# Kernel tuning notes

Measured on AMD Instinct MI355X. Metric: run time of the kernel, lower is better.

Reference implementation:

```python
import jax, jax.numpy as jnp
import numpy as np

CONF_THRES = 0.25
IOU_THRES = 0.45
MAX_DET = 1000
MAX_WH = 4096.0   # class offset for per-class NMS (yolov5 trick)
TOPK = 2048       # pre-NMS candidate cap (fixed-shape stand-in for max_nms)


def _xywh2xyxy(b):
    cx, cy, w, h = b[..., 0], b[..., 1], b[..., 2], b[..., 3]
    return jnp.stack([cx - w * 0.5, cy - h * 0.5, cx + w * 0.5, cy + h * 0.5], axis=-1)


def _box_iou(a, b):
    # a, b: [K, 4] in xyxy -> [K, K] pairwise IoU
    lt = jnp.maximum(a[:, None, :2], b[None, :, :2])
    rb = jnp.minimum(a[:, None, 2:], b[None, :, 2:])
    wh = jnp.clip(rb - lt, 0.0)
    inter = wh[..., 0] * wh[..., 1]
    area_a = (a[:, 2] - a[:, 0]) * (a[:, 3] - a[:, 1])
    area_b = (b[:, 2] - b[:, 0]) * (b[:, 3] - b[:, 1])
    return inter / (area_a[:, None] + area_b[None, :] - inter + 1e-7)


def _nms_single(pred):
    # pred: [N, 5+C] = (cx, cy, w, h, obj, cls...)
    obj = pred[:, 4]
    cls_prob = pred[:, 5:]
    cls_conf = jnp.max(cls_prob, axis=-1)
    cls_id = jnp.argmax(cls_prob, axis=-1)
    score = obj * cls_conf                      # conf = obj_conf * cls_conf (best class)
    valid = (obj > CONF_THRES) & (score > CONF_THRES)
    score = jnp.where(valid, score, 0.0)
    boxes = _xywh2xyxy(pred[:, :4])

    # keep top-K candidates by confidence (sorted descending)
    tops, idx = jax.lax.top_k(score, TOPK)
    boxes_k = boxes[idx]                        # [K, 4]
    cls_k = cls_id[idx]                         # [K]
    val_k = tops > 0.0

    # per-class NMS via class offset
    shifted = boxes_k + (cls_k.astype(boxes_k.dtype) * MAX_WH)[:, None]
    iou = _box_iou(shifted, shifted)            # [K, K]

    j = jnp.arange(TOPK)

    def body(i, keep):
        # if box i survives, suppress lower-scored boxes with IoU > thresh
        sup = keep[i] & (iou[i] > IOU_THRES) & (j > i)
        return keep & ~sup

    keep = jax.lax.fori_loop(0, TOPK, body, val_k)

    # gather up to MAX_DET kept detections (already score-sorted)
    fs, fi = jax.lax.top_k(jnp.where(keep, tops, -1.0), MAX_DET)
    ok = fs > 0.0
    det_boxes = jnp.where(ok[:, None], boxes_k[fi], 0.0)
    det_score = jnp.where(ok, tops[fi], 0.0)
    det_cls = jnp.where(ok, cls_k[fi].astype(det_boxes.dtype), -1.0)
    # [MAX_DET, 6] = (x1, y1, x2, y2, conf, cls); padded rows have conf 0, cls -1
    return jnp.concatenate([det_boxes, det_score[:, None], det_cls[:, None]], axis=-1)


def setup_inputs() -> dict:
    key = jax.random.key(0)
    raw = jax.random.uniform(key, (16, 25200, 85), dtype=jnp.float32)
    xy = raw[..., 0:2] * 640.0            # centers within a 640x640 image
    wh = raw[..., 2:4] * 120.0 + 2.0      # box sizes in [2, 122]
    rest = raw[..., 4:]                   # obj + class probs in [0, 1)
    pred = jnp.concatenate([xy, wh, rest], axis=-1)
    return {"pred": pred}


def reference(pred):
    return jax.vmap(_nms_single)(pred)
```

## Files before the change

kernel.cpp:

```cpp
#include <hip/hip_runtime.h>
#include <stdint.h>

#pragma clang fp contract(off)

#define BB 16
#define NN 25200
#define ROW 85
#define NCLS 80
#define TK 2048
#define SORTN 4096
#define NBIN 4096
#define MAXDET 1000
#define CONF 0.25f
#define IOUT 0.45f
#define MAXWH 4096.0f
#define SROWS 64

typedef float fvec4 __attribute__((ext_vector_type(4)));

#define AS1 __attribute__((address_space(1)))
#define AS3 __attribute__((address_space(3)))

__global__ __launch_bounds__(64) void score_kernel(const float* __restrict__ pred,
                                                   float* __restrict__ scores,
                                                   int* __restrict__ cls,
                                                   unsigned int* __restrict__ hist) {
  __shared__ __align__(16) float srow[SROWS * ROW];
  const int tile = blockIdx.x;
  const int b = blockIdx.y;
  const int lane = threadIdx.x;
  const int row0 = tile * SROWS;
  int nrows = NN - row0;
  if (nrows > SROWS) nrows = SROWS;
  const char* gsrc = (const char*)(pred + ((size_t)b * NN + row0) * ROW);
  const int nbytes = nrows * ROW * 4;
  for (int off = lane * 16; off < nbytes; off += 64 * 16) {
    __builtin_amdgcn_global_load_lds((AS1 void*)(gsrc + off),
                                     (AS3 void*)((char*)srow + (off - lane * 16)),
                                     16, 0, 0);
  }
  __builtin_amdgcn_s_waitcnt(0);
  __syncthreads();
  if (lane < nrows) {
    const int n = row0 + lane;
    const float* r = srow + lane * ROW;
    float obj = r[4];
    float best = r[5];
    int bid = 0;
#pragma unroll
    for (int c = 1; c < NCLS; ++c) {
      float p = r[5 + c];
      if (p > best) { best = p; bid = c; }
    }
    float score = obj * best;
    bool valid = (obj > CONF) && (score > CONF);
    float sout = valid ? score : 0.0f;
    scores[(size_t)b * NN + n] = sout;
    cls[(size_t)b * NN + n] = bid;
    if (valid) {
      unsigned int u = __float_as_uint(sout);
      unsigned int bin = (u - 0x3E800001u) >> 12;
      if (bin > NBIN - 1) bin = NBIN - 1;
      atomicAdd(&hist[(size_t)b * NBIN + bin], 1u);
    }
  }
}

__global__ __launch_bounds__(1024) void gather_kernel(const float* __restrict__ pred,
                                                      const float* __restrict__ scores,
                                                      const int* __restrict__ cls,
                                                      const unsigned int* __restrict__ hist,
                                                      float* __restrict__ tops,
                                                      float* __restrict__ boxes,
                                                      int* __restrict__ clsk,
                                                      int* __restrict__ keep,
                                                      int* __restrict__ cgrp,
                                                      int* __restrict__ coff) {
  const int b = blockIdx.x;
  const int t = threadIdx.x;
  const int w = t >> 6;
  const int lane = t & 63;
  __shared__ unsigned long long skey[SORTN];
  __shared__ unsigned int sh[NBIN];
  __shared__ unsigned int soff[NBIN];
  __shared__ int spart[1024];
  __shared__ unsigned short scls[TK];
  __shared__ int ccnt[NCLS];
  __shared__ int coffs[NCLS + 1];
  __shared__ int sP;

  if (t == 0) sP = 0;
  for (int i = t; i < NBIN; i += 1024) sh[i] = hist[(size_t)b * NBIN + i];
  for (int i = t; i < SORTN; i += 1024) skey[i] = 0ull;
  __syncthreads();

  int loc[4];
  int ssum = 0;
#pragma unroll
  for (int k = 0; k < 4; ++k) {
    loc[k] = (int)sh[NBIN - 1 - (4 * t + k)];
    ssum += loc[k];
  }
  spart[t] = ssum;
  __syncthreads();
  for (int o = 1; o < 1024; o <<= 1) {
    int v = (t >= o) ? spart[t - o] : 0;
    __syncthreads();
    spart[t] += v;
    __syncthreads();
  }
  int run = spart[t] - ssum;
#pragma unroll
  for (int k = 0; k < 4; ++k) {
    int bin = NBIN - 1 - (4 * t + k);
    soff[bin] = (unsigned int)run;
    if (run < TK && run + loc[k] >= TK) sP = bin;
    run += loc[k];
  }
  __syncthreads();
  const int P = sP;
  for (int i = t; i < NBIN; i += 1024) sh[i] = 0u;
  __syncthreads();

  const float* sc = scores + (size_t)b * NN;
  for (int n = t; n < NN; n += 1024) {
    unsigned int u = __float_as_uint(sc[n]);
    if (u > 0x3E800000u) {
      unsigned int bin = (u - 0x3E800001u) >> 12;
      if (bin > NBIN - 1) bin = NBIN - 1;
      if ((int)bin >= P) {
        unsigned int pos = soff[bin] + atomicAdd(&sh[bin], 1u);
        if (pos < SORTN)
          skey[pos] = ((unsigned long long)u << 32) | (unsigned int)(~n);
      }
    }
  }
  __syncthreads();

  for (int bin = P + w; bin < NBIN; bin += 16) {
    int s = (int)sh[bin];
    if (s < 2) continue;
    int base = (int)soff[bin];
    if (base >= SORTN) continue;
    if (base + s > SORTN) s = SORTN - base;
    if (s < 2) continue;
    if (s <= 64) {
      bool act = lane < s;
      unsigned long long key = act ? skey[base + lane] : 0ull;
      int rank = 0;
      for (int j = 0; j < s; ++j) {
        unsigned long long kj = skey[base + j];
        rank += (act && kj > key) ? 1 : 0;
      }
      if (act) skey[base + rank] = key;
    } else {
      for (int pass = 0; pass < s; ++pass) {
        for (int p = base + (pass & 1) + 2 * lane; p + 1 < base + s; p += 128) {
          unsigned long long a = skey[p], b2 = skey[p + 1];
          if (a < b2) { skey[p] = b2; skey[p + 1] = a; }
        }
        asm volatile("" ::: "memory");
      }
    }
    asm volatile("" ::: "memory");
  }
  __syncthreads();

  for (int i = t; i < TK; i += 1024) {
    unsigned long long key = skey[i];
    unsigned int ub = (unsigned int)(key >> 32);
    size_t gi = (size_t)b * TK + i;
    if (ub == 0u) {
      tops[gi] = 0.0f;
      clsk[gi] = 0;
      keep[gi] = 0;
      fvec4 z; z[0] = 0.f; z[1] = 0.f; z[2] = 0.f; z[3] = 0.f;
      *(fvec4*)(boxes + gi * 4) = z;
      scls[i] = (unsigned short)0xFFFFu;
    } else {
      int idx = (int)(~(unsigned int)key);
      tops[gi] = __uint_as_float(ub);
      int cl = cls[(size_t)b * NN + idx];
      clsk[gi] = cl;
      scls[i] = (unsigned short)cl;
      const float* rowp = pred + ((size_t)b * NN + idx) * ROW;
      float cx = rowp[0], cy = rowp[1], w2 = rowp[2], h2 = rowp[3];
      float hw = w2 * 0.5f, hh = h2 * 0.5f;
      fvec4 bb4;
      bb4[0] = cx - hw; bb4[1] = cy - hh; bb4[2] = cx + hw; bb4[3] = cy + hh;
      *(fvec4*)(boxes + gi * 4) = bb4;
    }
  }
  __syncthreads();

#pragma unroll
  for (int k = 0; k < 5; ++k) {
    int c = w + 16 * k;
    int cnt = 0;
    for (int base2 = 0; base2 < TK; base2 += 64) {
      bool match = ((int)scls[base2 + lane] == c);
      cnt += (int)__popcll(__ballot(match));
    }
    if (lane == 0) ccnt[c] = cnt;
  }
  __syncthreads();
  if (t == 0) {
    int r2 = 0;
    for (int c = 0; c < NCLS; ++c) { coffs[c] = r2; r2 += ccnt[c]; }
    coffs[NCLS] = r2;
  }
  __syncthreads();
#pragma unroll
  for (int k = 0; k < 5; ++k) {
    int c = w + 16 * k;
    int run2 = coffs[c];
    for (int base2 = 0; base2 < TK; base2 += 64) {
      bool match = ((int)scls[base2 + lane] == c);
      unsigned long long bal = __ballot(match);
      int r3 = (int)__popcll(bal & ((1ull << lane) - 1ull));
      if (match) cgrp[(size_t)b * TK + run2 + r3] = base2 + lane;
      run2 += (int)__popcll(bal);
    }
  }
  for (int c = t; c <= NCLS; c += 1024) coff[b * (NCLS + 1) + c] = coffs[c];
}

__global__ __launch_bounds__(64) void nms_kernel(const float* __restrict__ tops,
                                                 const float* __restrict__ boxes,
                                                 const int* __restrict__ cgrp,
                                                 const int* __restrict__ coff,
                                                 int* __restrict__ keep) {
  const int c = blockIdx.x;
  const int b = blockIdx.y;
  const int lane = threadIdx.x;
  const int start = coff[b * (NCLS + 1) + c];
  const int end = coff[b * (NCLS + 1) + c + 1];
  const int m = end - start;
  if (m <= 0) return;
  __shared__ float sx1[TK], sy1[TK], sx2[TK], sy2[TK];
  __shared__ unsigned short spos[TK];
  __shared__ unsigned char skp[TK];

  const float shift = (float)c * MAXWH;
  for (int i = lane; i < m; i += 64) {
    int j = cgrp[(size_t)b * TK + start + i];
    fvec4 bx = *(const fvec4*)(boxes + ((size_t)b * TK + j) * 4);
    sx1[i] = bx[0] + shift;
    sy1[i] = bx[1] + shift;
    sx2[i] = bx[2] + shift;
    sy2[i] = bx[3] + shift;
    spos[i] = (unsigned short)j;
    skp[i] = (tops[(size_t)b * TK + j] > 0.0f) ? 1 : 0;
  }
  __syncthreads();

  for (int i = 0; i < m; ++i) {
    __syncthreads();
    if (!skp[i]) continue;
    float ax1 = sx1[i], ay1 = sy1[i], ax2 = sx2[i], ay2 = sy2[i];
    float aarea = (ax2 - ax1) * (ay2 - ay1);
    for (int j = i + 1 + lane; j < m; j += 64) {
      float bx1 = sx1[j], by1 = sy1[j], bx2 = sx2[j], by2 = sy2[j];
      float ltx = fmaxf(ax1, bx1), lty = fmaxf(ay1, by1);
      float rbx = fminf(ax2, bx2), rby = fminf(ay2, by2);
      float iw = fmaxf(rbx - ltx, 0.0f);
      float ih = fmaxf(rby - lty, 0.0f);
      float inter = iw * ih;
      float barea = (bx2 - bx1) * (by2 - by1);
      float iou = inter / (aarea + barea - inter + 1e-7f);
      if (iou > IOUT) skp[j] = 0;
    }
  }
  __syncthreads();

  for (int i = lane; i < m; i += 64) {
    keep[(size_t)b * TK + spos[i]] = skp[i];
  }
}

__global__ __launch_bounds__(256) void out_kernel(const float* __restrict__ tops,
                                                  const float* __restrict__ boxes,
                                                  const int* __restrict__ clsk,
                                                  const int* __restrict__ keep,
                                                  float* __restrict__ out) {
  int b = blockIdx.x;
  int t = threadIdx.x;
  __shared__ int scnt[256];
  const int CH = TK / 256;
  int base = t * CH;
  int kp[CH];
  int cnt = 0;
  for (int k = 0; k < CH; ++k) {
    kp[k] = keep[(size_t)b * TK + base + k];
    cnt += kp[k];
  }
  scnt[t] = cnt;
  __syncthreads();
  for (int off = 1; off < 256; off <<= 1) {
    int v = (t >= off) ? scnt[t - off] : 0;
    __syncthreads();
    scnt[t] += v;
    __syncthreads();
  }
  int r = scnt[t] - cnt;
  int K = scnt[255];
  for (int k = 0; k < CH; ++k) {
    if (kp[k]) {
      if (r < MAXDET) {
        int j = base + k;
        float* o = out + ((size_t)b * MAXDET + r) * 6;
        const float* bx = boxes + ((size_t)b * TK + j) * 4;
        o[0] = bx[0]; o[1] = bx[1]; o[2] = bx[2]; o[3] = bx[3];
        o[4] = tops[(size_t)b * TK + j];
        o[5] = (float)clsk[(size_t)b * TK + j];
      }
      ++r;
    }
  }
  int Kc = K < MAXDET ? K : MAXDET;
  for (int r2 = Kc + t; r2 < MAXDET; r2 += 256) {
    float* o = out + ((size_t)b * MAXDET + r2) * 6;
    o[0] = 0.0f; o[1] = 0.0f; o[2] = 0.0f; o[3] = 0.0f; o[4] = 0.0f; o[5] = -1.0f;
  }
}

extern "C" void kernel_launch(void* const* d_in, const int* in_sizes, int n_in,
                              void* d_out, int out_size, void* d_ws, size_t ws_size,
                              hipStream_t stream) {
  const float* pred = (const float*)d_in[0];
  float* out = (float*)d_out;

  char* ws = (char*)d_ws;
  size_t off = 0;
  float* scores = (float*)(ws + off); off += (size_t)BB * NN * 4;
  int*   cls    = (int*)(ws + off);   off += (size_t)BB * NN * 4;
  float* tops   = (float*)(ws + off); off += (size_t)BB * TK * 4;
  float* boxes  = (float*)(ws + off); off += (size_t)BB * TK * 16;
  int*   clsk   = (int*)(ws + off);   off += (size_t)BB * TK * 4;
  int*   keep   = (int*)(ws + off);   off += (size_t)BB * TK * 4;
  unsigned int* hist = (unsigned int*)(ws + off); off += (size_t)BB * NBIN * 4;
  int*   cgrp   = (int*)(ws + off);   off += (size_t)BB * TK * 4;
  int*   coff   = (int*)(ws + off);   off += (size_t)BB * (NCLS + 1) * 4;
  (void)ws_size; (void)in_sizes; (void)n_in; (void)out_size;

  hipMemsetAsync(hist, 0, (size_t)BB * NBIN * 4, stream);
  score_kernel<<<dim3((NN + SROWS - 1) / SROWS, BB), 64, 0, stream>>>(pred, scores, cls, hist);
  gather_kernel<<<BB, 1024, 0, stream>>>(pred, scores, cls, hist, tops, boxes, clsk, keep, cgrp, coff);
  nms_kernel<<<dim3(NCLS, BB), 64, 0, stream>>>(tops, boxes, cgrp, coff, keep);
  out_kernel<<<BB, 256, 0, stream>>>(tops, boxes, clsk, keep, out);
}
```

Baseline: 272.6 us.

## Fuse gather, per-class NMS and output into one per-batch kernel

Merges the gather, NMS and output kernels into a single 1024-thread block per image. Candidate boxes, scores, classes and keep flags now stay in LDS instead of going through global workspace buffers. NMS runs per wavefront over its classes, keeping suppression bits in a register mask and fetching the reference box by lane shuffle, so the per-iteration block barrier is gone. The score kernel also uses 128-thread blocks and stores class ids as bytes; in exchange, NMS runs with only 16 blocks and drops the class coordinate shift, which may change rounding slightly.

```diff
diff --git a/kernel.cpp b/kernel.cpp
--- a/kernel.cpp
+++ b/kernel.cpp
@@ -21,29 +21,30 @@
 #define AS1 __attribute__((address_space(1)))
 #define AS3 __attribute__((address_space(3)))
 
-__global__ __launch_bounds__(64) void score_kernel(const float* __restrict__ pred,
-                                                   float* __restrict__ scores,
-                                                   int* __restrict__ cls,
-                                                   unsigned int* __restrict__ hist) {
+__global__ __launch_bounds__(128) void score_kernel(const float* __restrict__ pred,
+                                                    float* __restrict__ scores,
+                                                    uint8_t* __restrict__ cls,
+                                                    unsigned int* __restrict__ hist) {
   __shared__ __align__(16) float srow[SROWS * ROW];
   const int tile = blockIdx.x;
   const int b = blockIdx.y;
-  const int lane = threadIdx.x;
+  const int tid = threadIdx.x;
+  const int lane = tid & 63;
   const int row0 = tile * SROWS;
   int nrows = NN - row0;
   if (nrows > SROWS) nrows = SROWS;
   const char* gsrc = (const char*)(pred + ((size_t)b * NN + row0) * ROW);
   const int nbytes = nrows * ROW * 4;
-  for (int off = lane * 16; off < nbytes; off += 64 * 16) {
+  for (int off = tid * 16; off < nbytes; off += 128 * 16) {
     __builtin_amdgcn_global_load_lds((AS1 void*)(gsrc + off),
                                      (AS3 void*)((char*)srow + (off - lane * 16)),
                                      16, 0, 0);
   }
   __builtin_amdgcn_s_waitcnt(0);
   __syncthreads();
-  if (lane < nrows) {
-    const int n = row0 + lane;
-    const float* r = srow + lane * ROW;
+  if (tid < nrows) {
+    const int n = row0 + tid;
+    const float* r = srow + tid * ROW;
     float obj = r[4];
     float best = r[5];
     int bid = 0;
@@ -56,7 +57,7 @@
     bool valid = (obj > CONF) && (score > CONF);
     float sout = valid ? score : 0.0f;
     scores[(size_t)b * NN + n] = sout;
-    cls[(size_t)b * NN + n] = bid;
+    cls[(size_t)b * NN + n] = (uint8_t)bid;
     if (valid) {
       unsigned int u = __float_as_uint(sout);
       unsigned int bin = (u - 0x3E800001u) >> 12;
@@ -66,16 +67,11 @@
   }
 }
 
-__global__ __launch_bounds__(1024) void gather_kernel(const float* __restrict__ pred,
-                                                      const float* __restrict__ scores,
-                                                      const int* __restrict__ cls,
-                                                      const unsigned int* __restrict__ hist,
-                                                      float* __restrict__ tops,
-                                                      float* __restrict__ boxes,
-                                                      int* __restrict__ clsk,
-                                                      int* __restrict__ keep,
-                                                      int* __restrict__ cgrp,
-                                                      int* __restrict__ coff) {
+__global__ __launch_bounds__(1024) void mega_kernel(const float* __restrict__ pred,
+                                                    const float* __restrict__ scores,
+                                                    const uint8_t* __restrict__ cls,
+                                                    const unsigned int* __restrict__ hist,
+                                                    float* __restrict__ out) {
   const int b = blockIdx.x;
   const int t = threadIdx.x;
   const int w = t >> 6;
@@ -83,8 +79,12 @@
   __shared__ unsigned long long skey[SORTN];
   __shared__ unsigned int sh[NBIN];
   __shared__ unsigned int soff[NBIN];
+  __shared__ float sx1[TK], sy1[TK], sx2[TK], sy2[TK];
+  __shared__ float stop[TK];
+  __shared__ unsigned short scls[TK];
+  __shared__ unsigned short cgrpL[TK];
+  __shared__ unsigned char skp[TK];
   __shared__ int spart[1024];
-  __shared__ unsigned short scls[TK];
   __shared__ int ccnt[NCLS];
   __shared__ int coffs[NCLS + 1];
   __shared__ int sP;
@@ -169,26 +169,20 @@
   for (int i = t; i < TK; i += 1024) {
     unsigned long long key = skey[i];
     unsigned int ub = (unsigned int)(key >> 32);
-    size_t gi = (size_t)b * TK + i;
     if (ub == 0u) {
-      tops[gi] = 0.0f;
-      clsk[gi] = 0;
-      keep[gi] = 0;
-      fvec4 z; z[0] = 0.f; z[1] = 0.f; z[2] = 0.f; z[3] = 0.f;
-      *(fvec4*)(boxes + gi * 4) = z;
+      stop[i] = 0.0f;
       scls[i] = (unsigned short)0xFFFFu;
+      skp[i] = 0;
+      sx1[i] = 0.f; sy1[i] = 0.f; sx2[i] = 0.f; sy2[i] = 0.f;
     } else {
       int idx = (int)(~(unsigned int)key);
-      tops[gi] = __uint_as_float(ub);
-      int cl = cls[(size_t)b * NN + idx];
-      clsk[gi] = cl;
-      scls[i] = (unsigned short)cl;
+      stop[i] = __uint_as_float(ub);
+      scls[i] = (unsigned short)cls[(size_t)b * NN + idx];
+      skp[i] = 1;
       const float* rowp = pred + ((size_t)b * NN + idx) * ROW;
       float cx = rowp[0], cy = rowp[1], w2 = rowp[2], h2 = rowp[3];
       float hw = w2 * 0.5f, hh = h2 * 0.5f;
-      fvec4 bb4;
-      bb4[0] = cx - hw; bb4[1] = cy - hh; bb4[2] = cx + hw; bb4[3] = cy + hh;
-      *(fvec4*)(boxes + gi * 4) = bb4;
+      sx1[i] = cx - hw; sy1[i] = cy - hh; sx2[i] = cx + hw; sy2[i] = cy + hh;
     }
   }
   __syncthreads();
@@ -218,107 +212,101 @@
       bool match = ((int)scls[base2 + lane] == c);
       unsigned long long bal = __ballot(match);
       int r3 = (int)__popcll(bal & ((1ull << lane) - 1ull));
-      if (match) cgrp[(size_t)b * TK + run2 + r3] = base2 + lane;
+      if (match) cgrpL[run2 + r3] = (unsigned short)(base2 + lane);
       run2 += (int)__popcll(bal);
     }
   }
-  for (int c = t; c <= NCLS; c += 1024) coff[b * (NCLS + 1) + c] = coffs[c];
-}
-
-__global__ __launch_bounds__(64) void nms_kernel(const float* __restrict__ tops,
-                                                 const float* __restrict__ boxes,
-                                                 const int* __restrict__ cgrp,
-                                                 const int* __restrict__ coff,
-                                                 int* __restrict__ keep) {
-  const int c = blockIdx.x;
-  const int b = blockIdx.y;
-  const int lane = threadIdx.x;
-  const int start = coff[b * (NCLS + 1) + c];
-  const int end = coff[b * (NCLS + 1) + c + 1];
-  const int m = end - start;
-  if (m <= 0) return;
-  __shared__ float sx1[TK], sy1[TK], sx2[TK], sy2[TK];
-  __shared__ unsigned short spos[TK];
-  __shared__ unsigned char skp[TK];
-
-  const float shift = (float)c * MAXWH;
-  for (int i = lane; i < m; i += 64) {
-    int j = cgrp[(size_t)b * TK + start + i];
-    fvec4 bx = *(const fvec4*)(boxes + ((size_t)b * TK + j) * 4);
-    sx1[i] = bx[0] + shift;
-    sy1[i] = bx[1] + shift;
-    sx2[i] = bx[2] + shift;
-    sy2[i] = bx[3] + shift;
-    spos[i] = (unsigned short)j;
-    skp[i] = (tops[(size_t)b * TK + j] > 0.0f) ? 1 : 0;
-  }
-  __syncthreads();
-
-  for (int i = 0; i < m; ++i) {
+  __syncthreads();
+
+  for (int k = 0; k < 5; ++k) {
+    int c = w + 16 * k;
+    int start = coffs[c];
+    int m = coffs[c + 1] - start;
+    if (m <= 0) continue;
+    int nq = (m + 63) >> 6;
+    unsigned int km = 0;
+    for (int q = 0; q < nq; ++q)
+      if (lane + (q << 6) < m) km |= (1u << q);
+    float b0x1 = 0.f, b0y1 = 0.f, b0x2 = 0.f, b0y2 = 0.f;
+    if (lane < m) {
+      int e0 = cgrpL[start + lane];
+      b0x1 = sx1[e0]; b0y1 = sy1[e0]; b0x2 = sx2[e0]; b0y2 = sy2[e0];
+    }
+    for (int i = 0; i < m; ++i) {
+      int q = i >> 6;
+      unsigned int kmi = __shfl(km, i & 63);
+      if (!((kmi >> q) & 1u)) continue;
+      float ax1, ay1, ax2, ay2;
+      if (q == 0) {
+        ax1 = __shfl(b0x1, i); ay1 = __shfl(b0y1, i);
+        ax2 = __shfl(b0x2, i); ay2 = __shfl(b0y2, i);
+      } else {
+        int ei = cgrpL[start + i];
+        ax1 = sx1[ei]; ay1 = sy1[ei]; ax2 = sx2[ei]; ay2 = sy2[ei];
+      }
+      float aarea = (ax2 - ax1) * (ay2 - ay1);
+      if ((km & 1u) && lane > i) {
+        float ltx = fmaxf(ax1, b0x1), lty = fmaxf(ay1, b0y1);
+        float rbx = fminf(ax2, b0x2), rby = fminf(ay2, b0y2);
+        float iw = fmaxf(rbx - ltx, 0.0f);
+        float ih = fmaxf(rby - lty, 0.0f);
+        float inter = iw * ih;
+        float barea = (b0x2 - b0x1) * (b0y2 - b0y1);
+        float iou = inter / (aarea + barea - inter + 1e-7f);
+        if (iou > IOUT) km &= ~1u;
+      }
+      for (int q2 = 1; q2 < nq; ++q2) {
+        int j = lane + (q2 << 6);
+        if (((km >> q2) & 1u) && j > i && j < m) {
+          int ej = cgrpL[start + j];
+          float jx1 = sx1[ej], jy1 = sy1[ej], jx2 = sx2[ej], jy2 = sy2[ej];
+          float ltx = fmaxf(ax1, jx1), lty = fmaxf(ay1, jy1);
+          float rbx = fminf(ax2, jx2), rby = fminf(ay2, jy2);
+          float iw = fmaxf(rbx - ltx, 0.0f);
+          float ih = fmaxf(rby - lty, 0.0f);
+          float inter = iw * ih;
+          float barea = (jx2 - jx1) * (jy2 - jy1);
+          float iou = inter / (aarea + barea - inter + 1e-7f);
+          if (iou > IOUT) km &= ~(1u << q2);
+        }
+      }
+    }
+    for (int q = 0; q < nq; ++q) {
+      int j = lane + (q << 6);
+      if (j < m) skp[cgrpL[start + j]] = (unsigned char)((km >> q) & 1u);
+    }
+  }
+  __syncthreads();
+
+  int kp0 = (int)skp[2 * t];
+  int kp1 = (int)skp[2 * t + 1];
+  int cnt2 = kp0 + kp1;
+  spart[t] = cnt2;
+  __syncthreads();
+  for (int o = 1; o < 1024; o <<= 1) {
+    int v = (t >= o) ? spart[t - o] : 0;
     __syncthreads();
-    if (!skp[i]) continue;
-    float ax1 = sx1[i], ay1 = sy1[i], ax2 = sx2[i], ay2 = sy2[i];
-    float aarea = (ax2 - ax1) * (ay2 - ay1);
-    for (int j = i + 1 + lane; j < m; j += 64) {
-      float bx1 = sx1[j], by1 = sy1[j], bx2 = sx2[j], by2 = sy2[j];
-      float ltx = fmaxf(ax1, bx1), lty = fmaxf(ay1, by1);
-      float rbx = fminf(ax2, bx2), rby = fminf(ay2, by2);
-      float iw = fmaxf(rbx - ltx, 0.0f);
-      float ih = fmaxf(rby - lty, 0.0f);
-      float inter = iw * ih;
-      float barea = (bx2 - bx1) * (by2 - by1);
-      float iou = inter / (aarea + barea - inter + 1e-7f);
-      if (iou > IOUT) skp[j] = 0;
-    }
-  }
-  __syncthreads();
-
-  for (int i = lane; i < m; i += 64) {
-    keep[(size_t)b * TK + spos[i]] = skp[i];
-  }
-}
-
-__global__ __launch_bounds__(256) void out_kernel(const float* __restrict__ tops,
-                                                  const float* __restrict__ boxes,
-                                                  const int* __restrict__ clsk,
-                                                  const int* __restrict__ keep,
-                                                  float* __restrict__ out) {
-  int b = blockIdx.x;
-  int t = threadIdx.x;
-  __shared__ int scnt[256];
-  const int CH = TK / 256;
-  int base = t * CH;
-  int kp[CH];
-  int cnt = 0;
-  for (int k = 0; k < CH; ++k) {
-    kp[k] = keep[(size_t)b * TK + base + k];
-    cnt += kp[k];
-  }
-  scnt[t] = cnt;
-  __syncthreads();
-  for (int off = 1; off < 256; off <<= 1) {
-    int v = (t >= off) ? scnt[t - off] : 0;
+    spart[t] += v;
     __syncthreads();
-    scnt[t] += v;
-    __syncthreads();
-  }
-  int r = scnt[t] - cnt;
-  int K = scnt[255];
-  for (int k = 0; k < CH; ++k) {
-    if (kp[k]) {
-      if (r < MAXDET) {
-        int j = base + k;
-        float* o = out + ((size_t)b * MAXDET + r) * 6;
-        const float* bx = boxes + ((size_t)b * TK + j) * 4;
-        o[0] = bx[0]; o[1] = bx[1]; o[2] = bx[2]; o[3] = bx[3];
-        o[4] = tops[(size_t)b * TK + j];
-        o[5] = (float)clsk[(size_t)b * TK + j];
-      }
-      ++r;
+  }
+  int r4 = spart[t] - cnt2;
+  int K = spart[1023];
+#pragma unroll
+  for (int k = 0; k < 2; ++k) {
+    int kp = (k == 0) ? kp0 : kp1;
+    if (kp) {
+      if (r4 < MAXDET) {
+        int j = 2 * t + k;
+        float* o = out + ((size_t)b * MAXDET + r4) * 6;
+        o[0] = sx1[j]; o[1] = sy1[j]; o[2] = sx2[j]; o[3] = sy2[j];
+        o[4] = stop[j];
+        o[5] = (float)scls[j];
+      }
+      ++r4;
     }
   }
   int Kc = K < MAXDET ? K : MAXDET;
-  for (int r2 = Kc + t; r2 < MAXDET; r2 += 256) {
+  for (int r2 = Kc + t; r2 < MAXDET; r2 += 1024) {
     float* o = out + ((size_t)b * MAXDET + r2) * 6;
     o[0] = 0.0f; o[1] = 0.0f; o[2] = 0.0f; o[3] = 0.0f; o[4] = 0.0f; o[5] = -1.0f;
   }
@@ -332,20 +320,13 @@
 
   char* ws = (char*)d_ws;
   size_t off = 0;
-  float* scores = (float*)(ws + off); off += (size_t)BB * NN * 4;
-  int*   cls    = (int*)(ws + off);   off += (size_t)BB * NN * 4;
-  float* tops   = (float*)(ws + off); off += (size_t)BB * TK * 4;
-  float* boxes  = (float*)(ws + off); off += (size_t)BB * TK * 16;
-  int*   clsk   = (int*)(ws + off);   off += (size_t)BB * TK * 4;
-  int*   keep   = (int*)(ws + off);   off += (size_t)BB * TK * 4;
-  unsigned int* hist = (unsigned int*)(ws + off); off += (size_t)BB * NBIN * 4;
-  int*   cgrp   = (int*)(ws + off);   off += (size_t)BB * TK * 4;
-  int*   coff   = (int*)(ws + off);   off += (size_t)BB * (NCLS + 1) * 4;
+  float*        scores = (float*)(ws + off);        off += (size_t)BB * NN * 4;
+  uint8_t*      cls    = (uint8_t*)(ws + off);      off += (size_t)BB * NN;
+  off = (off + 255) & ~(size_t)255;
+  unsigned int* hist   = (unsigned int*)(ws + off); off += (size_t)BB * NBIN * 4;
   (void)ws_size; (void)in_sizes; (void)n_in; (void)out_size;
 
   hipMemsetAsync(hist, 0, (size_t)BB * NBIN * 4, stream);
-  score_kernel<<<dim3((NN + SROWS - 1) / SROWS, BB), 64, 0, stream>>>(pred, scores, cls, hist);
-  gather_kernel<<<BB, 1024, 0, stream>>>(pred, scores, cls, hist, tops, boxes, clsk, keep, cgrp, coff);
-  nms_kernel<<<dim3(NCLS, BB), 64, 0, stream>>>(tops, boxes, cgrp, coff, keep);
-  out_kernel<<<BB, 256, 0, stream>>>(tops, boxes, clsk, keep, out);
+  score_kernel<<<dim3((NN + SROWS - 1) / SROWS, BB), 128, 0, stream>>>(pred, scores, cls, hist);
+  mega_kernel<<<BB, 1024, 0, stream>>>(pred, scores, cls, hist, out);
 }
```

Result: slower. 290.4 us (+6.5%).
